# Kernel tuning notes

Measured on AMD Instinct MI355X. Metric: run time of the kernel, lower is better.

The kernel has to match this reference:

```python
import jax, jax.numpy as jnp
import numpy as np

N_NODES = 100000
N_EDGES = 3200000
NUM_GRAPHS = 64
IN_DIM = 256
HID = 64


def gcn_conv(x, W, b, src, dst, ew, n):
    # PyG GCNConv: add self-loops (weight 1), symmetric normalization,
    # out[dst] += norm * (x @ W)[src], then + bias.
    loop = jnp.arange(n, dtype=src.dtype)
    s = jnp.concatenate([src, loop])
    d = jnp.concatenate([dst, loop])
    w = jnp.concatenate([ew, jnp.ones((n,), dtype=ew.dtype)])
    deg = jax.ops.segment_sum(w, d, num_segments=n)
    dinv = jnp.where(deg > 0, jax.lax.rsqrt(jnp.where(deg > 0, deg, 1.0)), 0.0)
    norm = dinv[s] * w * dinv[d]  # [E+N]
    h = x @ W  # [N, out] transform before aggregation (cheaper messages)
    msg = h[s] * norm[:, None]  # [E+N, out]
    return jax.ops.segment_sum(msg, d, num_segments=n) + b


def setup_inputs() -> dict:
    key = jax.random.key(0)
    ks = jax.random.split(key, 10)
    x = jax.random.normal(ks[0], (N_NODES, IN_DIM), dtype=jnp.float32)
    edge_index = jax.random.randint(ks[1], (2, N_EDGES), 0, N_NODES, dtype=jnp.int64)
    edge_weight = jax.random.uniform(ks[2], (N_EDGES,), dtype=jnp.float32)
    batch = jnp.sort(jax.random.randint(ks[3], (N_NODES,), 0, NUM_GRAPHS, dtype=jnp.int64))
    W1 = jax.random.normal(ks[4], (IN_DIM, HID), dtype=jnp.float32) * (1.0 / np.sqrt(IN_DIM))
    b1 = jax.random.normal(ks[5], (HID,), dtype=jnp.float32) * 0.01
    W2 = jax.random.normal(ks[6], (HID, HID // 2), dtype=jnp.float32) * (1.0 / np.sqrt(HID))
    b2 = jax.random.normal(ks[7], (HID // 2,), dtype=jnp.float32) * 0.01
    Wlin = jax.random.normal(ks[8], (HID // 2, 4), dtype=jnp.float32) * (1.0 / np.sqrt(HID // 2))
    blin = jax.random.normal(ks[9], (4,), dtype=jnp.float32) * 0.01
    return {"x": x, "edge_index": edge_index, "edge_weight": edge_weight, "batch": batch,
            "W1": W1, "b1": b1, "W2": W2, "b2": b2, "Wlin": Wlin, "blin": blin}


def reference(x, edge_index, edge_weight, batch, W1, b1, W2, b2, Wlin, blin):
    src, dst = edge_index[0], edge_index[1]
    n = x.shape[0]
    h = jax.nn.relu(gcn_conv(x, W1, b1, src, dst, edge_weight, n))
    h = jax.nn.relu(gcn_conv(h, W2, b2, src, dst, edge_weight, n))
    pooled = jax.ops.segment_max(h, batch, num_segments=NUM_GRAPHS)  # [G, 32]
    return pooled @ Wlin + blin  # [G, 4]
```

## Files before the change

### kernel.cpp

```cpp
#include <hip/hip_runtime.h>
#include <hip/hip_bf16.h>


#define NTHREADS 256
#define SCAN_CHUNK 1024
#define NBP 512
#define BSHIFT 9

__device__ __forceinline__ unsigned short f2bf(float f) {
    unsigned int u = __float_as_uint(f);
    u = (u + 0x7FFFu + ((u >> 16) & 1u)) >> 16;
    return (unsigned short)u;
}
__device__ __forceinline__ float bf2f(unsigned short s) {
    return __uint_as_float((unsigned int)s << 16);
}

__global__ __launch_bounds__(NTHREADS) void p1_count_kernel(const int* __restrict__ dst,
                                                            unsigned int* __restrict__ cnt2d,
                                                            int nE, int nbuckets, int chunk) {
    __shared__ unsigned int hist[256];
    const int blk = blockIdx.x;
    const int t = threadIdx.x;
    hist[t] = 0;
    __syncthreads();
    const int e0 = blk * chunk;
    const int e1 = min(nE, e0 + chunk);
    for (int e = e0 + t; e < e1; e += NTHREADS)
        atomicAdd(&hist[dst[e] >> BSHIFT], 1u);
    __syncthreads();
    if (t < nbuckets) cnt2d[(size_t)t * NBP + blk] = hist[t];
}

__global__ __launch_bounds__(NTHREADS) void scan1_kernel(const unsigned int* __restrict__ in,
                                                         unsigned int* __restrict__ outv,
                                                         unsigned int* __restrict__ bsum, int n) {
    __shared__ unsigned int tmp[NTHREADS];
    const int base = blockIdx.x * SCAN_CHUNK;
    const int t = threadIdx.x;
    unsigned int v[4];
    #pragma unroll
    for (int k = 0; k < 4; ++k) {
        int i = base + t * 4 + k;
        v[k] = (i < n) ? in[i] : 0u;
    }
    unsigned int s = v[0] + v[1] + v[2] + v[3];
    tmp[t] = s;
    __syncthreads();
    for (int off = 1; off < NTHREADS; off <<= 1) {
        unsigned int val = (t >= off) ? tmp[t - off] : 0u;
        __syncthreads();
        tmp[t] += val;
        __syncthreads();
    }
    unsigned int excl = tmp[t] - s;
    if (t == NTHREADS - 1) bsum[blockIdx.x] = tmp[NTHREADS - 1];
    unsigned int run = excl;
    #pragma unroll
    for (int k = 0; k < 4; ++k) {
        int i = base + t * 4 + k;
        if (i < n) outv[i] = run;
        run += v[k];
    }
}

__global__ __launch_bounds__(NTHREADS) void scan2_kernel(unsigned int* __restrict__ bsum, int nb) {
    __shared__ unsigned int tmp[NTHREADS];
    int t = threadIdx.x;
    unsigned int v = (t < nb) ? bsum[t] : 0u;
    tmp[t] = v;
    __syncthreads();
    for (int off = 1; off < NTHREADS; off <<= 1) {
        unsigned int val = (t >= off) ? tmp[t - off] : 0u;
        __syncthreads();
        tmp[t] += val;
        __syncthreads();
    }
    if (t < nb) bsum[t] = tmp[t] - v;
}

__global__ __launch_bounds__(NTHREADS) void scan3_kernel(unsigned int* __restrict__ outv,
                                                         const unsigned int* __restrict__ bsum, int n) {
    int i = blockIdx.x * NTHREADS + threadIdx.x;
    if (i < n) outv[i] += bsum[i / SCAN_CHUNK];
}

__global__ __launch_bounds__(NTHREADS) void p2_scatter_kernel(const int* __restrict__ src,
                                                              const int* __restrict__ dst,
                                                              const float* __restrict__ ew,
                                                              const unsigned int* __restrict__ base2d,
                                                              int2* __restrict__ pairs,
                                                              int nE, int nbuckets, int chunk) {
    __shared__ unsigned int fill[256];
    const int blk = blockIdx.x;
    const int t = threadIdx.x;
    if (t < nbuckets) fill[t] = base2d[(size_t)t * NBP + blk];
    __syncthreads();
    const int e0 = blk * chunk;
    const int e1 = min(nE, e0 + chunk);
    for (int e = e0 + t; e < e1; e += NTHREADS) {
        int d = dst[e];
        int s = src[e];
        unsigned int q = (unsigned int)(ew[e] * 32768.0f + 0.5f);
        q = q > 32767u ? 32767u : q;
        unsigned int m = ((unsigned int)s << 15) | q;
        unsigned int pos = atomicAdd(&fill[d >> BSHIFT], 1u);
        pairs[pos] = make_int2(d, (int)m);
    }
}

__global__ __launch_bounds__(1024) void p3_csr_kernel(const int2* __restrict__ pairs,
                                                      const unsigned int* __restrict__ base2d,
                                                      unsigned int* __restrict__ meta,
                                                      int* __restrict__ rowptr,
                                                      float* __restrict__ dinv,
                                                      int n, int nE, int nbuckets) {
    __shared__ unsigned int cnt[512];
    __shared__ unsigned int wsum[512];
    __shared__ unsigned int sc[512];
    __shared__ unsigned int fillL[512];
    const int b = blockIdx.x;
    const int t = threadIdx.x;
    const int node0 = b << BSHIFT;
    const int nloc = min(512, n - node0);
    const unsigned int e0 = base2d[(size_t)b * NBP];
    const unsigned int e1 = (b + 1 < nbuckets) ? base2d[(size_t)(b + 1) * NBP] : (unsigned int)nE;

    if (t < 512) { cnt[t] = 0u; wsum[t] = 0u; }
    __syncthreads();

    for (unsigned int e = e0 + t; e < e1; e += 1024) {
        int2 p = pairs[e];
        int dl = p.x & 511;
        atomicAdd(&cnt[dl], 1u);
        atomicAdd(&wsum[dl], (unsigned int)(p.y & 32767));
    }
    __syncthreads();

    if (t < 512) sc[t] = cnt[t];
    __syncthreads();
    for (int off = 1; off < 512; off <<= 1) {
        unsigned int v = (t >= off && t < 512) ? sc[t - off] : 0u;
        __syncthreads();
        if (t < 512) sc[t] += v;
        __syncthreads();
    }
    if (t < nloc) {
        unsigned int ex = sc[t] - cnt[t];
        rowptr[node0 + t] = (int)(e0 + ex);
        fillL[t] = ex;
        dinv[node0 + t] = rsqrtf(1.0f + (float)wsum[t] * (1.0f / 32768.0f));
    }
    if (b == nbuckets - 1 && t == 0) rowptr[n] = nE;
    __syncthreads();

    for (unsigned int e = e0 + t; e < e1; e += 1024) {
        int2 p = pairs[e];
        int dl = p.x & 511;
        unsigned int pos = e0 + atomicAdd(&fillL[dl], 1u);
        meta[pos] = (unsigned int)p.y;
    }
}

__global__ __launch_bounds__(NTHREADS) void gemm1_kernel(const float* __restrict__ x,
                                                         const float* __restrict__ W,
                                                         const float* __restrict__ dinv,
                                                         unsigned short* __restrict__ g, int n) {
    __shared__ float xT[32][132];
    __shared__ float ws[32][64];
    const int t = threadIdx.x;
    const int row0 = blockIdx.x * 128;
    const int tc4 = (t & 15) * 4;
    const int tr8 = (t >> 4) * 8;
    const int kq = (t & 7) * 4;
    const int rsub = t >> 3;
    float acc[8][4] = {};

    for (int kb = 0; kb < 256; kb += 32) {
        #pragma unroll
        for (int p = 0; p < 4; ++p) {
            int r = p * 32 + rsub;
            int grow = row0 + r;
            float4 v = make_float4(0.f, 0.f, 0.f, 0.f);
            if (grow < n) v = *(const float4*)&x[(size_t)grow * 256 + kb + kq];
            xT[kq + 0][r] = v.x; xT[kq + 1][r] = v.y;
            xT[kq + 2][r] = v.z; xT[kq + 3][r] = v.w;
        }
        #pragma unroll
        for (int p = 0; p < 2; ++p) {
            int k = p * 16 + (t >> 4);
            *(float4*)&ws[k][tc4] = *(const float4*)&W[(size_t)(kb + k) * 64 + tc4];
        }
        __syncthreads();
        #pragma unroll
        for (int kk = 0; kk < 32; ++kk) {
            float4 wv = *(const float4*)&ws[kk][tc4];
            float4 xa = *(const float4*)&xT[kk][tr8];
            float4 xb = *(const float4*)&xT[kk][tr8 + 4];
            float xr[8] = {xa.x, xa.y, xa.z, xa.w, xb.x, xb.y, xb.z, xb.w};
            #pragma unroll
            for (int r = 0; r < 8; ++r) {
                acc[r][0] = fmaf(xr[r], wv.x, acc[r][0]);
                acc[r][1] = fmaf(xr[r], wv.y, acc[r][1]);
                acc[r][2] = fmaf(xr[r], wv.z, acc[r][2]);
                acc[r][3] = fmaf(xr[r], wv.w, acc[r][3]);
            }
        }
        __syncthreads();
    }
    #pragma unroll
    for (int r = 0; r < 8; ++r) {
        int grow = row0 + tr8 + r;
        if (grow < n) {
            float di = dinv[grow];
            ushort4 o;
            o.x = f2bf(di * acc[r][0]); o.y = f2bf(di * acc[r][1]);
            o.z = f2bf(di * acc[r][2]); o.w = f2bf(di * acc[r][3]);
            *(ushort4*)&g[(size_t)grow * 64 + tc4] = o;
        }
    }
}

__global__ __launch_bounds__(NTHREADS) void agg1_csr_kernel(const int* __restrict__ rowptr,
                                                            const unsigned int* __restrict__ meta,
                                                            const unsigned short* __restrict__ g1,
                                                            const float* __restrict__ dinv,
                                                            const float* __restrict__ b1,
                                                            float* __restrict__ y1, int n) {
    const int wid = (blockIdx.x * NTHREADS + threadIdx.x) >> 6;
    if (wid >= n) return;
    const int l = threadIdx.x & 63;
    const int fg = l & 15, eg = l >> 4;
    const int j4 = fg * 4;
    const int beg = rowptr[wid], end = rowptr[wid + 1];
    const float di = dinv[wid];
    const ushort4 su = *(const ushort4*)&g1[(size_t)wid * 64 + j4];

    float4 acc = make_float4(0.f, 0.f, 0.f, 0.f);
    int k = beg + eg;
    for (; k + 4 < end; k += 8) {
        unsigned int m0 = meta[k];
        unsigned int m1 = meta[k + 4];
        ushort4 u0 = *(const ushort4*)&g1[(size_t)(m0 >> 15) * 64 + j4];
        ushort4 u1 = *(const ushort4*)&g1[(size_t)(m1 >> 15) * 64 + j4];
        float w0 = (float)(m0 & 32767u) * (1.0f / 32768.0f);
        float w1 = (float)(m1 & 32767u) * (1.0f / 32768.0f);
        acc.x = fmaf(w0, bf2f(u0.x), acc.x); acc.y = fmaf(w0, bf2f(u0.y), acc.y);
        acc.z = fmaf(w0, bf2f(u0.z), acc.z); acc.w = fmaf(w0, bf2f(u0.w), acc.w);
        acc.x = fmaf(w1, bf2f(u1.x), acc.x); acc.y = fmaf(w1, bf2f(u1.y), acc.y);
        acc.z = fmaf(w1, bf2f(u1.z), acc.z); acc.w = fmaf(w1, bf2f(u1.w), acc.w);
    }
    if (k < end) {
        unsigned int m = meta[k];
        ushort4 u = *(const ushort4*)&g1[(size_t)(m >> 15) * 64 + j4];
        float w = (float)(m & 32767u) * (1.0f / 32768.0f);
        acc.x = fmaf(w, bf2f(u.x), acc.x); acc.y = fmaf(w, bf2f(u.y), acc.y);
        acc.z = fmaf(w, bf2f(u.z), acc.z); acc.w = fmaf(w, bf2f(u.w), acc.w);
    }
    #pragma unroll
    for (int m = 16; m <= 32; m <<= 1) {
        acc.x += __shfl_xor(acc.x, m);
        acc.y += __shfl_xor(acc.y, m);
        acc.z += __shfl_xor(acc.z, m);
        acc.w += __shfl_xor(acc.w, m);
    }
    if (eg == 0) {
        float4 bb = *(const float4*)&b1[j4];
        float4 r;
        r.x = fmaxf(fmaf(di, acc.x + bf2f(su.x), bb.x), 0.f);
        r.y = fmaxf(fmaf(di, acc.y + bf2f(su.y), bb.y), 0.f);
        r.z = fmaxf(fmaf(di, acc.z + bf2f(su.z), bb.z), 0.f);
        r.w = fmaxf(fmaf(di, acc.w + bf2f(su.w), bb.w), 0.f);
        *(float4*)&y1[(size_t)wid * 64 + j4] = r;
    }
}

__global__ __launch_bounds__(NTHREADS) void gemm2_kernel(const float* __restrict__ y1,
                                                         const float* __restrict__ W,
                                                         const float* __restrict__ dinv,
                                                         unsigned short* __restrict__ g, int n) {
    __shared__ float xT[64][68];
    __shared__ float ws[64][32];
    const int t = threadIdx.x;
    const int row0 = blockIdx.x * 64;
    const int tc2 = (t & 15) * 2;
    const int tr4 = (t >> 4) * 4;
    float acc[4][2] = {};

    const int tx = t & 63;
    const int ty = t >> 6;
    #pragma unroll
    for (int rp = 0; rp < 16; ++rp) {
        int r = ty * 16 + rp;
        int grow = row0 + r;
        float v = (grow < n) ? y1[(size_t)grow * 64 + tx] : 0.0f;
        xT[tx][r] = v;
    }
    #pragma unroll
    for (int p = 0; p < 8; ++p) {
        int idx = p * 256 + t;
        ws[idx >> 5][idx & 31] = W[idx];
    }
    __syncthreads();
    #pragma unroll
    for (int kk = 0; kk < 64; ++kk) {
        float4 xv = *(const float4*)&xT[kk][tr4];
        float2 wv = *(const float2*)&ws[kk][tc2];
        acc[0][0] += xv.x * wv.x; acc[0][1] += xv.x * wv.y;
        acc[1][0] += xv.y * wv.x; acc[1][1] += xv.y * wv.y;
        acc[2][0] += xv.z * wv.x; acc[2][1] += xv.z * wv.y;
        acc[3][0] += xv.w * wv.x; acc[3][1] += xv.w * wv.y;
    }
    #pragma unroll
    for (int r = 0; r < 4; ++r) {
        int grow = row0 + tr4 + r;
        if (grow < n) {
            float di = dinv[grow];
            ushort2 o;
            o.x = f2bf(di * acc[r][0]); o.y = f2bf(di * acc[r][1]);
            *(ushort2*)&g[(size_t)grow * 32 + tc2] = o;
        }
    }
}

__global__ __launch_bounds__(NTHREADS) void agg2_csr_pool_kernel(const int* __restrict__ rowptr,
                                                                 const unsigned int* __restrict__ meta,
                                                                 const unsigned short* __restrict__ g2,
                                                                 const float* __restrict__ dinv,
                                                                 const float* __restrict__ b2,
                                                                 const int* __restrict__ batch,
                                                                 unsigned int* __restrict__ pooled,
                                                                 int n) {
    __shared__ float smax[4][32];
    __shared__ int sb[4];
    const int w = threadIdx.x >> 6;
    const int l = threadIdx.x & 63;
    const int node = blockIdx.x * 4 + w;
    const bool active = node < n;
    const int fg = l & 7, eg = l >> 3;
    const int j4 = fg * 4;

    if (l == 0) sb[w] = active ? batch[node] : -1;

    if (active) {
        const int beg = rowptr[node], end = rowptr[node + 1];
        const float di = dinv[node];
        const ushort4 su = *(const ushort4*)&g2[(size_t)node * 32 + j4];

        float4 acc = make_float4(0.f, 0.f, 0.f, 0.f);
        int k = beg + eg;
        for (; k + 8 < end; k += 16) {
            unsigned int m0 = meta[k];
            unsigned int m1 = meta[k + 8];
            ushort4 u0 = *(const ushort4*)&g2[(size_t)(m0 >> 15) * 32 + j4];
            ushort4 u1 = *(const ushort4*)&g2[(size_t)(m1 >> 15) * 32 + j4];
            float w0 = (float)(m0 & 32767u) * (1.0f / 32768.0f);
            float w1 = (float)(m1 & 32767u) * (1.0f / 32768.0f);
            acc.x = fmaf(w0, bf2f(u0.x), acc.x); acc.y = fmaf(w0, bf2f(u0.y), acc.y);
            acc.z = fmaf(w0, bf2f(u0.z), acc.z); acc.w = fmaf(w0, bf2f(u0.w), acc.w);
            acc.x = fmaf(w1, bf2f(u1.x), acc.x); acc.y = fmaf(w1, bf2f(u1.y), acc.y);
            acc.z = fmaf(w1, bf2f(u1.z), acc.z); acc.w = fmaf(w1, bf2f(u1.w), acc.w);
        }
        if (k < end) {
            unsigned int m = meta[k];
            ushort4 u = *(const ushort4*)&g2[(size_t)(m >> 15) * 32 + j4];
            float wq = (float)(m & 32767u) * (1.0f / 32768.0f);
            acc.x = fmaf(wq, bf2f(u.x), acc.x); acc.y = fmaf(wq, bf2f(u.y), acc.y);
            acc.z = fmaf(wq, bf2f(u.z), acc.z); acc.w = fmaf(wq, bf2f(u.w), acc.w);
        }
        #pragma unroll
        for (int m = 8; m <= 32; m <<= 1) {
            acc.x += __shfl_xor(acc.x, m);
            acc.y += __shfl_xor(acc.y, m);
            acc.z += __shfl_xor(acc.z, m);
            acc.w += __shfl_xor(acc.w, m);
        }
        if (eg == 0) {
            float4 bb = *(const float4*)&b2[j4];
            float4 r;
            r.x = fmaxf(fmaf(di, acc.x + bf2f(su.x), bb.x), 0.f);
            r.y = fmaxf(fmaf(di, acc.y + bf2f(su.y), bb.y), 0.f);
            r.z = fmaxf(fmaf(di, acc.z + bf2f(su.z), bb.z), 0.f);
            r.w = fmaxf(fmaf(di, acc.w + bf2f(su.w), bb.w), 0.f);
            *(float4*)&smax[w][j4] = r;
        }
    }
    __syncthreads();
    const int t = threadIdx.x;
    if (t < 32) {
        int b0 = sb[0], b1_ = sb[1], b2_ = sb[2], b3_ = sb[3];
        if (b0 >= 0 && b0 == b1_ && b0 == b2_ && b0 == b3_) {
            float v = fmaxf(fmaxf(smax[0][t], smax[1][t]), fmaxf(smax[2][t], smax[3][t]));
            atomicMax(&pooled[b0 * 32 + t], __float_as_uint(v));
        } else {
            #pragma unroll
            for (int ww = 0; ww < 4; ++ww) {
                if (sb[ww] >= 0)
                    atomicMax(&pooled[sb[ww] * 32 + t], __float_as_uint(smax[ww][t]));
            }
        }
    }
}

__global__ __launch_bounds__(NTHREADS) void final_kernel(const float* __restrict__ pooled,
                                                         const float* __restrict__ Wlin,
                                                         const float* __restrict__ blin,
                                                         float* __restrict__ out) {
    int t = threadIdx.x;
    int g = t >> 2, c = t & 3;
    float s = blin[c];
    #pragma unroll
    for (int j = 0; j < 32; ++j) s += pooled[g * 32 + j] * Wlin[j * 4 + c];
    out[g * 4 + c] = s;
}

extern "C" void kernel_launch(void* const* d_in, const int* in_sizes, int n_in,
                              void* d_out, int out_size, void* d_ws, size_t ws_size,
                              hipStream_t stream) {
    const float* x     = (const float*)d_in[0];
    const int*   ei    = (const int*)d_in[1];
    const float* ew    = (const float*)d_in[2];
    const int*   batch = (const int*)d_in[3];
    const float* W1    = (const float*)d_in[4];
    const float* b1    = (const float*)d_in[5];
    const float* W2    = (const float*)d_in[6];
    const float* b2    = (const float*)d_in[7];
    const float* Wlin  = (const float*)d_in[8];
    const float* blin  = (const float*)d_in[9];
    float* out = (float*)d_out;

    const int E = in_sizes[2];
    const int n = in_sizes[3];
    const int* src = ei;
    const int* dst = ei + E;

    const int nbuckets = (n + 511) >> BSHIFT;
    const int chunk = (E + NBP - 1) / NBP;
    const int scanlen = nbuckets * NBP;
    const int nchunks = (scanlen + SCAN_CHUNK - 1) / SCAN_CHUNK;

    auto al = [](size_t v) { return (v + 63) & ~(size_t)63; };
    float* ws = (float*)d_ws;
    size_t off = 0;
    unsigned int* cnt2d  = (unsigned int*)(ws + off); off += al(scanlen);
    unsigned int* base2d = (unsigned int*)(ws + off); off += al(scanlen);
    unsigned int* bsum   = (unsigned int*)(ws + off); off += al(256);
    float* dinv    = ws + off; off += al(n);
    int*   rowptr  = (int*)(ws + off); off += al(n + 1);
    unsigned int* meta = (unsigned int*)(ws + off); off += al(E);
    unsigned short* g1 = (unsigned short*)(ws + off); off += al((size_t)n * 32);
    float* y1      = ws + off; off += al((size_t)n * 64);
    float* pooled  = ws + off; off += al(64 * 32);
    unsigned short* g2 = g1;
    int2*  pairs = (int2*)y1;

    hipMemsetAsync(pooled, 0, 64 * 32 * sizeof(float), stream);

    p1_count_kernel<<<NBP, NTHREADS, 0, stream>>>(dst, cnt2d, E, nbuckets, chunk);
    scan1_kernel<<<nchunks, NTHREADS, 0, stream>>>(cnt2d, base2d, bsum, scanlen);
    scan2_kernel<<<1, NTHREADS, 0, stream>>>(bsum, nchunks);
    scan3_kernel<<<(scanlen + 255) / 256, NTHREADS, 0, stream>>>(base2d, bsum, scanlen);
    p2_scatter_kernel<<<NBP, NTHREADS, 0, stream>>>(src, dst, ew, base2d, pairs, E, nbuckets, chunk);
    p3_csr_kernel<<<nbuckets, 1024, 0, stream>>>(pairs, base2d, meta, rowptr, dinv, n, E, nbuckets);

    gemm1_kernel<<<(n + 127) / 128, NTHREADS, 0, stream>>>(x, W1, dinv, g1, n);
    agg1_csr_kernel<<<(n + 3) / 4, NTHREADS, 0, stream>>>(rowptr, meta, g1, dinv, b1, y1, n);

    gemm2_kernel<<<(n + 63) / 64, NTHREADS, 0, stream>>>(y1, W2, dinv, g2, n);
    agg2_csr_pool_kernel<<<(n + 3) / 4, NTHREADS, 0, stream>>>(
        rowptr, meta, g2, dinv, b2, batch, (unsigned int*)pooled, n);

    final_kernel<<<1, NTHREADS, 0, stream>>>(pooled, Wlin, blin, out);
}
```

Baseline: 503.2 us.

## Stage bucket scatter in LDS, store layer-1 activations as bf16, unroll gathers

The edge scatter kernel now sorts each chunk's edges by bucket in shared memory and then writes them to global memory in contiguous runs, instead of scattering single elements with atomics straight to global. The hidden activation y1 is stored as bf16 instead of fp32, which halves its write and read traffic between agg1 and gemm2. Both aggregation loops are unrolled to four gathers per iteration to raise memory-level parallelism. The trade-offs are about 56KB of shared memory per scatter block, which lowers occupancy, an extra bf16 rounding step on y1, and a separate pairs buffer in the workspace.

```diff
diff --git a/kernel.cpp b/kernel.cpp
--- a/kernel.cpp
+++ b/kernel.cpp
@@ -6,6 +6,7 @@
 #define SCAN_CHUNK 1024
 #define NBP 512
 #define BSHIFT 9
+#define MAXCHUNK 6272
 
 __device__ __forceinline__ unsigned short f2bf(float f) {
     unsigned int u = __float_as_uint(f);
@@ -88,24 +89,54 @@
 __global__ __launch_bounds__(NTHREADS) void p2_scatter_kernel(const int* __restrict__ src,
                                                               const int* __restrict__ dst,
                                                               const float* __restrict__ ew,
+                                                              const unsigned int* __restrict__ cnt2d,
                                                               const unsigned int* __restrict__ base2d,
                                                               int2* __restrict__ pairs,
                                                               int nE, int nbuckets, int chunk) {
+    __shared__ int2 stage[MAXCHUNK];
+    __shared__ unsigned char stgb[MAXCHUNK];
+    __shared__ unsigned int lofs[256];
     __shared__ unsigned int fill[256];
+    __shared__ unsigned int gbase[256];
     const int blk = blockIdx.x;
     const int t = threadIdx.x;
-    if (t < nbuckets) fill[t] = base2d[(size_t)t * NBP + blk];
-    __syncthreads();
+
+    unsigned int c = (t < nbuckets) ? cnt2d[(size_t)t * NBP + blk] : 0u;
+    lofs[t] = c;
+    if (t < nbuckets) gbase[t] = base2d[(size_t)t * NBP + blk];
+    __syncthreads();
+    for (int off = 1; off < NTHREADS; off <<= 1) {
+        unsigned int val = (t >= off) ? lofs[t - off] : 0u;
+        __syncthreads();
+        lofs[t] += val;
+        __syncthreads();
+    }
+    unsigned int ex = lofs[t] - c;
+    __syncthreads();
+    lofs[t] = ex;
+    fill[t] = ex;
+    __syncthreads();
+
     const int e0 = blk * chunk;
     const int e1 = min(nE, e0 + chunk);
     for (int e = e0 + t; e < e1; e += NTHREADS) {
         int d = dst[e];
         int s = src[e];
+        int b = d >> BSHIFT;
         unsigned int q = (unsigned int)(ew[e] * 32768.0f + 0.5f);
         q = q > 32767u ? 32767u : q;
         unsigned int m = ((unsigned int)s << 15) | q;
-        unsigned int pos = atomicAdd(&fill[d >> BSHIFT], 1u);
-        pairs[pos] = make_int2(d, (int)m);
+        unsigned int slot = atomicAdd(&fill[b], 1u);
+        stage[slot] = make_int2(d, (int)m);
+        stgb[slot] = (unsigned char)b;
+    }
+    __syncthreads();
+
+    const int total = e1 - e0;
+    for (int i = t; i < total; i += NTHREADS) {
+        int b = stgb[i];
+        unsigned int gpos = gbase[b] + ((unsigned int)i - lofs[b]);
+        pairs[gpos] = stage[i];
     }
 }
 
@@ -226,7 +257,7 @@
                                                             const unsigned short* __restrict__ g1,
                                                             const float* __restrict__ dinv,
                                                             const float* __restrict__ b1,
-                                                            float* __restrict__ y1, int n) {
+                                                            unsigned short* __restrict__ y1, int n) {
     const int wid = (blockIdx.x * NTHREADS + threadIdx.x) >> 6;
     if (wid >= n) return;
     const int l = threadIdx.x & 63;
@@ -238,19 +269,29 @@
 
     float4 acc = make_float4(0.f, 0.f, 0.f, 0.f);
     int k = beg + eg;
-    for (; k + 4 < end; k += 8) {
+    for (; k + 12 < end; k += 16) {
         unsigned int m0 = meta[k];
         unsigned int m1 = meta[k + 4];
+        unsigned int m2 = meta[k + 8];
+        unsigned int m3 = meta[k + 12];
         ushort4 u0 = *(const ushort4*)&g1[(size_t)(m0 >> 15) * 64 + j4];
         ushort4 u1 = *(const ushort4*)&g1[(size_t)(m1 >> 15) * 64 + j4];
+        ushort4 u2 = *(const ushort4*)&g1[(size_t)(m2 >> 15) * 64 + j4];
+        ushort4 u3 = *(const ushort4*)&g1[(size_t)(m3 >> 15) * 64 + j4];
         float w0 = (float)(m0 & 32767u) * (1.0f / 32768.0f);
         float w1 = (float)(m1 & 32767u) * (1.0f / 32768.0f);
+        float w2 = (float)(m2 & 32767u) * (1.0f / 32768.0f);
+        float w3 = (float)(m3 & 32767u) * (1.0f / 32768.0f);
         acc.x = fmaf(w0, bf2f(u0.x), acc.x); acc.y = fmaf(w0, bf2f(u0.y), acc.y);
         acc.z = fmaf(w0, bf2f(u0.z), acc.z); acc.w = fmaf(w0, bf2f(u0.w), acc.w);
         acc.x = fmaf(w1, bf2f(u1.x), acc.x); acc.y = fmaf(w1, bf2f(u1.y), acc.y);
         acc.z = fmaf(w1, bf2f(u1.z), acc.z); acc.w = fmaf(w1, bf2f(u1.w), acc.w);
-    }
-    if (k < end) {
+        acc.x = fmaf(w2, bf2f(u2.x), acc.x); acc.y = fmaf(w2, bf2f(u2.y), acc.y);
+        acc.z = fmaf(w2, bf2f(u2.z), acc.z); acc.w = fmaf(w2, bf2f(u2.w), acc.w);
+        acc.x = fmaf(w3, bf2f(u3.x), acc.x); acc.y = fmaf(w3, bf2f(u3.y), acc.y);
+        acc.z = fmaf(w3, bf2f(u3.z), acc.z); acc.w = fmaf(w3, bf2f(u3.w), acc.w);
+    }
+    for (; k < end; k += 4) {
         unsigned int m = meta[k];
         ushort4 u = *(const ushort4*)&g1[(size_t)(m >> 15) * 64 + j4];
         float w = (float)(m & 32767u) * (1.0f / 32768.0f);
@@ -266,16 +307,16 @@
     }
     if (eg == 0) {
         float4 bb = *(const float4*)&b1[j4];
-        float4 r;
-        r.x = fmaxf(fmaf(di, acc.x + bf2f(su.x), bb.x), 0.f);
-        r.y = fmaxf(fmaf(di, acc.y + bf2f(su.y), bb.y), 0.f);
-        r.z = fmaxf(fmaf(di, acc.z + bf2f(su.z), bb.z), 0.f);
-        r.w = fmaxf(fmaf(di, acc.w + bf2f(su.w), bb.w), 0.f);
-        *(float4*)&y1[(size_t)wid * 64 + j4] = r;
-    }
-}
-
-__global__ __launch_bounds__(NTHREADS) void gemm2_kernel(const float* __restrict__ y1,
+        ushort4 o;
+        o.x = f2bf(fmaxf(fmaf(di, acc.x + bf2f(su.x), bb.x), 0.f));
+        o.y = f2bf(fmaxf(fmaf(di, acc.y + bf2f(su.y), bb.y), 0.f));
+        o.z = f2bf(fmaxf(fmaf(di, acc.z + bf2f(su.z), bb.z), 0.f));
+        o.w = f2bf(fmaxf(fmaf(di, acc.w + bf2f(su.w), bb.w), 0.f));
+        *(ushort4*)&y1[(size_t)wid * 64 + j4] = o;
+    }
+}
+
+__global__ __launch_bounds__(NTHREADS) void gemm2_kernel(const unsigned short* __restrict__ y1,
                                                          const float* __restrict__ W,
                                                          const float* __restrict__ dinv,
                                                          unsigned short* __restrict__ g, int n) {
@@ -293,7 +334,7 @@
     for (int rp = 0; rp < 16; ++rp) {
         int r = ty * 16 + rp;
         int grow = row0 + r;
-        float v = (grow < n) ? y1[(size_t)grow * 64 + tx] : 0.0f;
+        float v = (grow < n) ? bf2f(y1[(size_t)grow * 64 + tx]) : 0.0f;
         xT[tx][r] = v;
     }
     #pragma unroll
@@ -349,19 +390,29 @@
 
         float4 acc = make_float4(0.f, 0.f, 0.f, 0.f);
         int k = beg + eg;
-        for (; k + 8 < end; k += 16) {
+        for (; k + 24 < end; k += 32) {
             unsigned int m0 = meta[k];
             unsigned int m1 = meta[k + 8];
+            unsigned int m2 = meta[k + 16];
+            unsigned int m3 = meta[k + 24];
             ushort4 u0 = *(const ushort4*)&g2[(size_t)(m0 >> 15) * 32 + j4];
             ushort4 u1 = *(const ushort4*)&g2[(size_t)(m1 >> 15) * 32 + j4];
+            ushort4 u2 = *(const ushort4*)&g2[(size_t)(m2 >> 15) * 32 + j4];
+            ushort4 u3 = *(const ushort4*)&g2[(size_t)(m3 >> 15) * 32 + j4];
             float w0 = (float)(m0 & 32767u) * (1.0f / 32768.0f);
             float w1 = (float)(m1 & 32767u) * (1.0f / 32768.0f);
+            float w2 = (float)(m2 & 32767u) * (1.0f / 32768.0f);
+            float w3 = (float)(m3 & 32767u) * (1.0f / 32768.0f);
             acc.x = fmaf(w0, bf2f(u0.x), acc.x); acc.y = fmaf(w0, bf2f(u0.y), acc.y);
             acc.z = fmaf(w0, bf2f(u0.z), acc.z); acc.w = fmaf(w0, bf2f(u0.w), acc.w);
             acc.x = fmaf(w1, bf2f(u1.x), acc.x); acc.y = fmaf(w1, bf2f(u1.y), acc.y);
             acc.z = fmaf(w1, bf2f(u1.z), acc.z); acc.w = fmaf(w1, bf2f(u1.w), acc.w);
-        }
-        if (k < end) {
+            acc.x = fmaf(w2, bf2f(u2.x), acc.x); acc.y = fmaf(w2, bf2f(u2.y), acc.y);
+            acc.z = fmaf(w2, bf2f(u2.z), acc.z); acc.w = fmaf(w2, bf2f(u2.w), acc.w);
+            acc.x = fmaf(w3, bf2f(u3.x), acc.x); acc.y = fmaf(w3, bf2f(u3.y), acc.y);
+            acc.z = fmaf(w3, bf2f(u3.z), acc.z); acc.w = fmaf(w3, bf2f(u3.w), acc.w);
+        }
+        for (; k < end; k += 8) {
             unsigned int m = meta[k];
             ushort4 u = *(const ushort4*)&g2[(size_t)(m >> 15) * 32 + j4];
             float wq = (float)(m & 32767u) * (1.0f / 32768.0f);
@@ -449,10 +500,10 @@
     int*   rowptr  = (int*)(ws + off); off += al(n + 1);
     unsigned int* meta = (unsigned int*)(ws + off); off += al(E);
     unsigned short* g1 = (unsigned short*)(ws + off); off += al((size_t)n * 32);
-    float* y1      = ws + off; off += al((size_t)n * 64);
+    unsigned short* y1 = (unsigned short*)(ws + off); off += al((size_t)n * 32);
+    int2*  pairs   = (int2*)(ws + off); off += al((size_t)E * 2);
     float* pooled  = ws + off; off += al(64 * 32);
     unsigned short* g2 = g1;
-    int2*  pairs = (int2*)y1;
 
     hipMemsetAsync(pooled, 0, 64 * 32 * sizeof(float), stream);
 
@@ -460,7 +511,7 @@
     scan1_kernel<<<nchunks, NTHREADS, 0, stream>>>(cnt2d, base2d, bsum, scanlen);
     scan2_kernel<<<1, NTHREADS, 0, stream>>>(bsum, nchunks);
     scan3_kernel<<<(scanlen + 255) / 256, NTHREADS, 0, stream>>>(base2d, bsum, scanlen);
-    p2_scatter_kernel<<<NBP, NTHREADS, 0, stream>>>(src, dst, ew, base2d, pairs, E, nbuckets, chunk);
+    p2_scatter_kernel<<<NBP, NTHREADS, 0, stream>>>(src, dst, ew, cnt2d, base2d, pairs, E, nbuckets, chunk);
     p3_csr_kernel<<<nbuckets, 1024, 0, stream>>>(pairs, base2d, meta, rowptr, dinv, n, E, nbuckets);
 
     gemm1_kernel<<<(n + 127) / 128, NTHREADS, 0, stream>>>(x, W1, dinv, g1, n);
```

Measured after the change: 480.1 us. 4.6% less time.
